# Performance work log

Hardware: AMD Instinct MI355X
Metric: run time of the kernel (lower is better)

The kernel has to match this reference:

```python
import jax, jax.numpy as jnp
import numpy as np

N = 512          # width of every layer (dims = [N]*4)
C = 16           # synaptic channels
NLAYERS = 4      # len(dims)
LT = NLAYERS - 1 # layer transitions
B = NLAYERS + N  # bias_vector_size = len(dims) + max(dims)
AGG_IN = N + B   # aggregator input width


def setup_inputs() -> dict:
    key = jax.random.key(0)
    ks = jax.random.split(key, 11)
    f32 = jnp.float32
    def rn(k, shape, scale):
        return (jax.random.normal(k, shape, f32) * scale)
    return {
        "x":      jax.random.normal(ks[0], (N,), f32),
        # Single_VECs: Linear(1, C) per (post q, pre p)
        "vec_W":  rn(ks[1], (LT, N, N, C), 1.0),
        "vec_b":  rn(ks[2], (LT, N, N, C), 0.5),
        # Single_Synapse: Linear(C,3) -> tanh -> Linear(3,1) -> tanh, per (q,p)
        "syn_W1": rn(ks[3], (LT, N, N, 3, C), 1.0 / np.sqrt(C)),
        "syn_b1": rn(ks[4], (LT, N, N, 3), 0.1),
        "syn_W2": rn(ks[5], (LT, N, N, 3), 1.0 / np.sqrt(3.0)),
        "syn_b2": rn(ks[6], (LT, N, N), 0.1),
        # Node_Aggregator: Linear(N + B, 3) -> tanh -> Linear(3,1), per q
        "agg_W1": rn(ks[7], (LT, N, 3, AGG_IN), 1.0 / np.sqrt(AGG_IN)),
        "agg_b1": rn(ks[8], (LT, N, 3), 0.1),
        "agg_W2": rn(ks[9], (LT, N, 3), 1.0 / np.sqrt(3.0)),
        "agg_b2": rn(ks[10], (LT, N), 0.1),
    }


def reference(x, vec_W, vec_b, syn_W1, syn_b1, syn_W2, syn_b2,
              agg_W1, agg_b1, agg_W2, agg_b2):
    # layer code for destination layer l+1 (one-hot over NLAYERS)
    layer_codes = jnp.eye(NLAYERS, dtype=x.dtype)[1:1 + LT]   # [LT, NLAYERS]
    node_eye = jnp.eye(N, dtype=x.dtype)                       # node one-hot codes

    def step(a, p):
        vW, vb, sW1, sb1, sW2, sb2, aW1, ab1, aW2, ab2, lcode = p
        # VECs: tanh(Linear(1->C)) per edge; a[p] is the scalar pre-activation
        filtered = jnp.tanh(a[None, :, None] * vW + vb)                 # [N_post, N_pre, C]
        # Single_Synapse per edge
        h1 = jnp.tanh(jnp.einsum('qpoc,qpc->qpo', sW1, filtered) + sb1) # [q, p, 3]
        s = jnp.tanh(jnp.einsum('qpo,qpo->qp', sW2, h1) + sb2)          # [q, p]
        # Node_Aggregator over cat(synapse_activations, bias_vector)
        agg_in = jnp.concatenate(
            [s, jnp.broadcast_to(lcode, (N, NLAYERS)), node_eye], axis=1)  # [q, N+B]
        h = jnp.tanh(jnp.einsum('qkp,qp->qk', aW1, agg_in) + ab1)       # [q, 3]
        a_next = jnp.einsum('qk,qk->q', aW2, h) + ab2                   # [q] (no tanh on fc2)
        return a_next, None

    a_final, _ = jax.lax.scan(
        step, x,
        (vec_W, vec_b, syn_W1, syn_b1, syn_W2, syn_b2,
         agg_W1, agg_b1, agg_W2, agg_b2, layer_codes))
    # original prepends each node: net_out = [node_{N-1}, ..., node_0], shape [N, 1]
    return a_final[::-1].reshape(-1, 1)
```

## Files before the change

### kernel.cpp

```cpp
#include <hip/hip_runtime.h>
#include <math.h>

#define N 512
#define C 16
#define NLAYERS 4
#define AGG_IN 1028

__global__ __launch_bounds__(512) void dan_layer_kernel(
    const float* __restrict__ a_in,
    float*       __restrict__ a_out,
    const float* __restrict__ vec_W,
    const float* __restrict__ vec_b,
    const float* __restrict__ syn_W1,
    const float* __restrict__ syn_b1,
    const float* __restrict__ syn_W2,
    const float* __restrict__ syn_b2,
    const float* __restrict__ agg_W1,
    const float* __restrict__ agg_b1,
    const float* __restrict__ agg_W2,
    const float* __restrict__ agg_b2,
    int l, int reverse_out)
{
    const int q = blockIdx.x;
    const int p = threadIdx.x;

    __shared__ float red[3][8];

    const size_t edge = ((size_t)(l * N + q)) * N + p;
    const float av = a_in[p];

    const float4* vW = (const float4*)(vec_W + edge * C);
    const float4* vB = (const float4*)(vec_b + edge * C);
    float f[16];
    #pragma unroll
    for (int j = 0; j < 4; ++j) {
        float4 w = vW[j];
        float4 b = vB[j];
        f[4*j+0] = tanhf(fmaf(av, w.x, b.x));
        f[4*j+1] = tanhf(fmaf(av, w.y, b.y));
        f[4*j+2] = tanhf(fmaf(av, w.z, b.z));
        f[4*j+3] = tanhf(fmaf(av, w.w, b.w));
    }

    const float4* sW1 = (const float4*)(syn_W1 + edge * 48);
    float h1[3];
    #pragma unroll
    for (int o = 0; o < 3; ++o) {
        float acc = syn_b1[edge * 3 + o];
        #pragma unroll
        for (int j = 0; j < 4; ++j) {
            float4 w = sW1[o * 4 + j];
            acc = fmaf(w.x, f[4*j+0], acc);
            acc = fmaf(w.y, f[4*j+1], acc);
            acc = fmaf(w.z, f[4*j+2], acc);
            acc = fmaf(w.w, f[4*j+3], acc);
        }
        h1[o] = tanhf(acc);
    }
    float s = syn_b2[edge];
    s = fmaf(syn_W2[edge*3+0], h1[0], s);
    s = fmaf(syn_W2[edge*3+1], h1[1], s);
    s = fmaf(syn_W2[edge*3+2], h1[2], s);
    s = tanhf(s);

    const float* aW1 = agg_W1 + ((size_t)(l * N + q)) * 3 * AGG_IN;
    float part0 = aW1[0 * AGG_IN + p] * s;
    float part1 = aW1[1 * AGG_IN + p] * s;
    float part2 = aW1[2 * AGG_IN + p] * s;

    #pragma unroll
    for (int off = 32; off > 0; off >>= 1) {
        part0 += __shfl_down(part0, off, 64);
        part1 += __shfl_down(part1, off, 64);
        part2 += __shfl_down(part2, off, 64);
    }
    const int wave = threadIdx.x >> 6;
    if ((threadIdx.x & 63) == 0) {
        red[0][wave] = part0;
        red[1][wave] = part1;
        red[2][wave] = part2;
    }
    __syncthreads();

    if (threadIdx.x == 0) {
        float h[3];
        #pragma unroll
        for (int k = 0; k < 3; ++k) {
            float acc = 0.f;
            #pragma unroll
            for (int w = 0; w < 8; ++w) acc += red[k][w];
            acc += aW1[k * AGG_IN + N + (l + 1)];
            acc += aW1[k * AGG_IN + N + NLAYERS + q];
            acc += agg_b1[((size_t)(l * N + q)) * 3 + k];
            h[k] = tanhf(acc);
        }
        const float* aW2 = agg_W2 + ((size_t)(l * N + q)) * 3;
        float out = agg_b2[l * N + q];
        out = fmaf(aW2[0], h[0], out);
        out = fmaf(aW2[1], h[1], out);
        out = fmaf(aW2[2], h[2], out);
        if (reverse_out) a_out[N - 1 - q] = out;
        else             a_out[q] = out;
    }
}

extern "C" void kernel_launch(void* const* d_in, const int* in_sizes, int n_in,
                              void* d_out, int out_size, void* d_ws, size_t ws_size,
                              hipStream_t stream) {
    const float* x      = (const float*)d_in[0];
    const float* vec_W  = (const float*)d_in[1];
    const float* vec_b  = (const float*)d_in[2];
    const float* syn_W1 = (const float*)d_in[3];
    const float* syn_b1 = (const float*)d_in[4];
    const float* syn_W2 = (const float*)d_in[5];
    const float* syn_b2 = (const float*)d_in[6];
    const float* agg_W1 = (const float*)d_in[7];
    const float* agg_b1 = (const float*)d_in[8];
    const float* agg_W2 = (const float*)d_in[9];
    const float* agg_b2 = (const float*)d_in[10];
    float* out = (float*)d_out;

    float* a0 = (float*)d_ws;
    float* a1 = a0 + N;

    dan_layer_kernel<<<N, N, 0, stream>>>(x,  a0,  vec_W, vec_b, syn_W1, syn_b1,
                                          syn_W2, syn_b2, agg_W1, agg_b1, agg_W2, agg_b2,
                                          0, 0);
    dan_layer_kernel<<<N, N, 0, stream>>>(a0, a1,  vec_W, vec_b, syn_W1, syn_b1,
                                          syn_W2, syn_b2, agg_W1, agg_b1, agg_W2, agg_b2,
                                          1, 0);
    dan_layer_kernel<<<N, N, 0, stream>>>(a1, out, vec_W, vec_b, syn_W1, syn_b1,
                                          syn_W2, syn_b2, agg_W1, agg_b1, agg_W2, agg_b2,
                                          2, 1);
}
```

Before: 336.2 us.

## Split edges across four lanes with atomic partials and fast tanh

Each edge's 16 channels are now spread over four lanes, so a thread loads one float4 of each weight row, and the 3-output dot product is combined with xor shuffles. Per-layer work is split into an edge kernel on an 8x512 grid that atomically accumulates aggregator partials into a zeroed workspace, followed by a single-block epilogue. tanhf is replaced by an exp-based fast_tanh. The goal is more coalesced, wider-parallel loads on this memory-bound weight stream, at the cost of extra launches, atomics, and a small loss of tanh accuracy.

```diff
diff --git a/kernel.cpp b/kernel.cpp
--- a/kernel.cpp
+++ b/kernel.cpp
@@ -3,12 +3,23 @@
 
 #define N 512
 #define C 16
-#define NLAYERS 4
+#define LT 3
 #define AGG_IN 1028
 
-__global__ __launch_bounds__(512) void dan_layer_kernel(
+__device__ __forceinline__ float fast_tanh(float x) {
+    float ax = fabsf(x);
+    float t  = __expf(-2.0f * ax);
+    float r  = __fdividef(1.0f - t, 1.0f + t);
+    return copysignf(r, x);
+}
+
+__global__ __launch_bounds__(512) void zero_partials(float* __restrict__ part, int n) {
+    int i = blockIdx.x * blockDim.x + threadIdx.x;
+    if (i < n) part[i] = 0.f;
+}
+
+__global__ __launch_bounds__(256) void edge_kernel(
     const float* __restrict__ a_in,
-    float*       __restrict__ a_out,
     const float* __restrict__ vec_W,
     const float* __restrict__ vec_b,
     const float* __restrict__ syn_W1,
@@ -16,92 +27,99 @@
     const float* __restrict__ syn_W2,
     const float* __restrict__ syn_b2,
     const float* __restrict__ agg_W1,
+    float* __restrict__ part,
+    int l)
+{
+    const int q  = blockIdx.y;
+    const int pc = blockIdx.x;
+    const int t  = threadIdx.x;
+    const int e  = t >> 2;
+    const int j  = t & 3;
+    const int p  = pc * 64 + e;
+
+    const size_t edge = ((size_t)(l * N + q)) * N + p;
+
+    const float av = a_in[p];
+
+    const float4 w = ((const float4*)(vec_W + edge * C))[j];
+    const float4 b = ((const float4*)(vec_b + edge * C))[j];
+
+    float4 f;
+    f.x = fast_tanh(fmaf(av, w.x, b.x));
+    f.y = fast_tanh(fmaf(av, w.y, b.y));
+    f.z = fast_tanh(fmaf(av, w.z, b.z));
+    f.w = fast_tanh(fmaf(av, w.w, b.w));
+
+    const float4* sW1 = (const float4*)(syn_W1 + edge * 48);
+    float d0, d1, d2;
+    {
+        float4 wv = sW1[0 * 4 + j];
+        d0 = fmaf(wv.x, f.x, fmaf(wv.y, f.y, fmaf(wv.z, f.z, wv.w * f.w)));
+        wv = sW1[1 * 4 + j];
+        d1 = fmaf(wv.x, f.x, fmaf(wv.y, f.y, fmaf(wv.z, f.z, wv.w * f.w)));
+        wv = sW1[2 * 4 + j];
+        d2 = fmaf(wv.x, f.x, fmaf(wv.y, f.y, fmaf(wv.z, f.z, wv.w * f.w)));
+    }
+    d0 += __shfl_xor(d0, 1, 64);  d0 += __shfl_xor(d0, 2, 64);
+    d1 += __shfl_xor(d1, 1, 64);  d1 += __shfl_xor(d1, 2, 64);
+    d2 += __shfl_xor(d2, 1, 64);  d2 += __shfl_xor(d2, 2, 64);
+
+    float h0 = fast_tanh(d0 + syn_b1[edge * 3 + 0]);
+    float h1 = fast_tanh(d1 + syn_b1[edge * 3 + 1]);
+    float h2 = fast_tanh(d2 + syn_b1[edge * 3 + 2]);
+    float s = syn_b2[edge];
+    s = fmaf(syn_W2[edge * 3 + 0], h0, s);
+    s = fmaf(syn_W2[edge * 3 + 1], h1, s);
+    s = fmaf(syn_W2[edge * 3 + 2], h2, s);
+    s = fast_tanh(s);
+
+    float pv = 0.f;
+    if (j < 3) {
+        pv = s * agg_W1[(((size_t)(l * N + q)) * 3 + j) * AGG_IN + p];
+    }
+    pv += __shfl_xor(pv, 4, 64);
+    pv += __shfl_xor(pv, 8, 64);
+    pv += __shfl_xor(pv, 16, 64);
+    pv += __shfl_xor(pv, 32, 64);
+
+    __shared__ float red[3][4];
+    const int wave = t >> 6;
+    const int lane = t & 63;
+    if (lane < 3) red[lane][wave] = pv;
+    __syncthreads();
+    if (t < 3) {
+        float acc = red[t][0] + red[t][1] + red[t][2] + red[t][3];
+        atomicAdd(&part[q * 3 + t], acc);
+    }
+}
+
+__global__ __launch_bounds__(512) void agg_epilogue(
+    const float* __restrict__ part,
+    const float* __restrict__ agg_W1,
     const float* __restrict__ agg_b1,
     const float* __restrict__ agg_W2,
     const float* __restrict__ agg_b2,
+    float* __restrict__ a_out,
     int l, int reverse_out)
 {
-    const int q = blockIdx.x;
-    const int p = threadIdx.x;
-
-    __shared__ float red[3][8];
-
-    const size_t edge = ((size_t)(l * N + q)) * N + p;
-    const float av = a_in[p];
-
-    const float4* vW = (const float4*)(vec_W + edge * C);
-    const float4* vB = (const float4*)(vec_b + edge * C);
-    float f[16];
+    const int q = threadIdx.x;
+    const float* aW1 = agg_W1 + ((size_t)(l * N + q)) * 3 * AGG_IN;
+    float h[3];
     #pragma unroll
-    for (int j = 0; j < 4; ++j) {
-        float4 w = vW[j];
-        float4 b = vB[j];
-        f[4*j+0] = tanhf(fmaf(av, w.x, b.x));
-        f[4*j+1] = tanhf(fmaf(av, w.y, b.y));
-        f[4*j+2] = tanhf(fmaf(av, w.z, b.z));
-        f[4*j+3] = tanhf(fmaf(av, w.w, b.w));
+    for (int k = 0; k < 3; ++k) {
+        float acc = part[q * 3 + k];
+        acc += aW1[k * AGG_IN + N + (l + 1)];
+        acc += aW1[k * AGG_IN + N + 4 + q];
+        acc += agg_b1[((size_t)(l * N + q)) * 3 + k];
+        h[k] = fast_tanh(acc);
     }
-
-    const float4* sW1 = (const float4*)(syn_W1 + edge * 48);
-    float h1[3];
-    #pragma unroll
-    for (int o = 0; o < 3; ++o) {
-        float acc = syn_b1[edge * 3 + o];
-        #pragma unroll
-        for (int j = 0; j < 4; ++j) {
-            float4 w = sW1[o * 4 + j];
-            acc = fmaf(w.x, f[4*j+0], acc);
-            acc = fmaf(w.y, f[4*j+1], acc);
-            acc = fmaf(w.z, f[4*j+2], acc);
-            acc = fmaf(w.w, f[4*j+3], acc);
-        }
-        h1[o] = tanhf(acc);
-    }
-    float s = syn_b2[edge];
-    s = fmaf(syn_W2[edge*3+0], h1[0], s);
-    s = fmaf(syn_W2[edge*3+1], h1[1], s);
-    s = fmaf(syn_W2[edge*3+2], h1[2], s);
-    s = tanhf(s);
-
-    const float* aW1 = agg_W1 + ((size_t)(l * N + q)) * 3 * AGG_IN;
-    float part0 = aW1[0 * AGG_IN + p] * s;
-    float part1 = aW1[1 * AGG_IN + p] * s;
-    float part2 = aW1[2 * AGG_IN + p] * s;
-
-    #pragma unroll
-    for (int off = 32; off > 0; off >>= 1) {
-        part0 += __shfl_down(part0, off, 64);
-        part1 += __shfl_down(part1, off, 64);
-        part2 += __shfl_down(part2, off, 64);
-    }
-    const int wave = threadIdx.x >> 6;
-    if ((threadIdx.x & 63) == 0) {
-        red[0][wave] = part0;
-        red[1][wave] = part1;
-        red[2][wave] = part2;
-    }
-    __syncthreads();
-
-    if (threadIdx.x == 0) {
-        float h[3];
-        #pragma unroll
-        for (int k = 0; k < 3; ++k) {
-            float acc = 0.f;
-            #pragma unroll
-            for (int w = 0; w < 8; ++w) acc += red[k][w];
-            acc += aW1[k * AGG_IN + N + (l + 1)];
-            acc += aW1[k * AGG_IN + N + NLAYERS + q];
-            acc += agg_b1[((size_t)(l * N + q)) * 3 + k];
-            h[k] = tanhf(acc);
-        }
-        const float* aW2 = agg_W2 + ((size_t)(l * N + q)) * 3;
-        float out = agg_b2[l * N + q];
-        out = fmaf(aW2[0], h[0], out);
-        out = fmaf(aW2[1], h[1], out);
-        out = fmaf(aW2[2], h[2], out);
-        if (reverse_out) a_out[N - 1 - q] = out;
-        else             a_out[q] = out;
-    }
+    const float* aW2 = agg_W2 + ((size_t)(l * N + q)) * 3;
+    float out = agg_b2[l * N + q];
+    out = fmaf(aW2[0], h[0], out);
+    out = fmaf(aW2[1], h[1], out);
+    out = fmaf(aW2[2], h[2], out);
+    if (reverse_out) a_out[N - 1 - q] = out;
+    else             a_out[q] = out;
 }
 
 extern "C" void kernel_launch(void* const* d_in, const int* in_sizes, int n_in,
@@ -120,16 +138,29 @@
     const float* agg_b2 = (const float*)d_in[10];
     float* out = (float*)d_out;
 
-    float* a0 = (float*)d_ws;
-    float* a1 = a0 + N;
+    float* part = (float*)d_ws;
+    float* a0   = part + LT * N * 3;
+    float* a1   = a0 + N;
 
-    dan_layer_kernel<<<N, N, 0, stream>>>(x,  a0,  vec_W, vec_b, syn_W1, syn_b1,
-                                          syn_W2, syn_b2, agg_W1, agg_b1, agg_W2, agg_b2,
-                                          0, 0);
-    dan_layer_kernel<<<N, N, 0, stream>>>(a0, a1,  vec_W, vec_b, syn_W1, syn_b1,
-                                          syn_W2, syn_b2, agg_W1, agg_b1, agg_W2, agg_b2,
-                                          1, 0);
-    dan_layer_kernel<<<N, N, 0, stream>>>(a1, out, vec_W, vec_b, syn_W1, syn_b1,
-                                          syn_W2, syn_b2, agg_W1, agg_b1, agg_W2, agg_b2,
-                                          2, 1);
+    zero_partials<<<(LT * N * 3 + 511) / 512, 512, 0, stream>>>(part, LT * N * 3);
+
+    const dim3 egrid(8, N);
+
+    edge_kernel<<<egrid, 256, 0, stream>>>(x, vec_W, vec_b, syn_W1, syn_b1,
+                                           syn_W2, syn_b2, agg_W1,
+                                           part + 0 * N * 3, 0);
+    agg_epilogue<<<1, N, 0, stream>>>(part + 0 * N * 3, agg_W1, agg_b1, agg_W2,
+                                      agg_b2, a0, 0, 0);
+
+    edge_kernel<<<egrid, 256, 0, stream>>>(a0, vec_W, vec_b, syn_W1, syn_b1,
+                                           syn_W2, syn_b2, agg_W1,
+                                           part + 1 * N * 3, 1);
+    agg_epilogue<<<1, N, 0, stream>>>(part + 1 * N * 3, agg_W1, agg_b1, agg_W2,
+                                      agg_b2, a1, 1, 0);
+
+    edge_kernel<<<egrid, 256, 0, stream>>>(a1, vec_W, vec_b, syn_W1, syn_b1,
+                                           syn_W2, syn_b2, agg_W1,
+                                           part + 2 * N * 3, 2);
+    agg_epilogue<<<1, N, 0, stream>>>(part + 2 * N * 3, agg_W1, agg_b1, agg_W2,
+                                      agg_b2, out, 2, 1);
 }
```

Result: slower. 347.7 us (+3.4%).

## Split each edge across four lanes with coalesced nontemporal loads and fast tanh

Applied to the files above, without the earlier changes.

Remaps threads so four lanes cooperate on one edge, each loading a 16-byte slice of the vec and synapse weights. A wave's loads become contiguous, and the 16-wide dot products are combined with intra-quad shuffles. Each block loops over four passes of 128 edges. Libm tanhf is replaced with an exp-based fast tanh, and loads are marked nontemporal. The fast tanh trades some accuracy, and the extra shuffles add ALU work.

```diff
diff --git a/kernel.cpp b/kernel.cpp
--- a/kernel.cpp
+++ b/kernel.cpp
@@ -3,10 +3,22 @@
 
 #define N 512
 #define C 16
-#define NLAYERS 4
 #define AGG_IN 1028
 
-__global__ __launch_bounds__(512) void dan_layer_kernel(
+typedef float v4f __attribute__((ext_vector_type(4)));
+
+__device__ __forceinline__ float fast_tanh(float x) {
+    float ax = fabsf(x);
+    float t  = __expf(-2.0f * ax);
+    float r  = __fdividef(1.0f - t, 1.0f + t);
+    return copysignf(r, x);
+}
+
+__device__ __forceinline__ v4f ntload4(const float* p) {
+    return __builtin_nontemporal_load((const v4f*)p);
+}
+
+__global__ __launch_bounds__(512, 4) void dan_layer_kernel(
     const float* __restrict__ a_in,
     float*       __restrict__ a_out,
     const float* __restrict__ vec_W,
@@ -22,83 +34,85 @@
     int l, int reverse_out)
 {
     const int q = blockIdx.x;
-    const int p = threadIdx.x;
+    const int t = threadIdx.x;
+    const int j = t & 3;
+    const int e = t >> 2;
 
     __shared__ float red[3][8];
+    __shared__ float hsh[3];
 
-    const size_t edge = ((size_t)(l * N + q)) * N + p;
-    const float av = a_in[p];
+    const size_t qbase = ((size_t)(l * N + q)) * N;
+    const int jc = (j < 3) ? j : 2;
+    const float* aW1q = agg_W1 + ((size_t)(l * N + q)) * 3 * AGG_IN + (size_t)jc * AGG_IN;
 
-    const float4* vW = (const float4*)(vec_W + edge * C);
-    const float4* vB = (const float4*)(vec_b + edge * C);
-    float f[16];
-    #pragma unroll
-    for (int j = 0; j < 4; ++j) {
-        float4 w = vW[j];
-        float4 b = vB[j];
-        f[4*j+0] = tanhf(fmaf(av, w.x, b.x));
-        f[4*j+1] = tanhf(fmaf(av, w.y, b.y));
-        f[4*j+2] = tanhf(fmaf(av, w.z, b.z));
-        f[4*j+3] = tanhf(fmaf(av, w.w, b.w));
+    float pv = 0.f;
+
+    for (int pass = 0; pass < 4; ++pass) {
+        const int p = pass * 128 + e;
+        const size_t edge = qbase + p;
+
+        const float av = a_in[p];
+
+        const v4f w  = ntload4(vec_W  + edge * C  + j * 4);
+        const v4f b  = ntload4(vec_b  + edge * C  + j * 4);
+        const v4f s0 = ntload4(syn_W1 + edge * 48 + 0 * C + j * 4);
+        const v4f s1 = ntload4(syn_W1 + edge * 48 + 1 * C + j * 4);
+        const v4f s2 = ntload4(syn_W1 + edge * 48 + 2 * C + j * 4);
+
+        float f0 = fast_tanh(fmaf(av, w.x, b.x));
+        float f1 = fast_tanh(fmaf(av, w.y, b.y));
+        float f2 = fast_tanh(fmaf(av, w.z, b.z));
+        float f3 = fast_tanh(fmaf(av, w.w, b.w));
+
+        float d0 = fmaf(s0.x, f0, fmaf(s0.y, f1, fmaf(s0.z, f2, s0.w * f3)));
+        float d1 = fmaf(s1.x, f0, fmaf(s1.y, f1, fmaf(s1.z, f2, s1.w * f3)));
+        float d2 = fmaf(s2.x, f0, fmaf(s2.y, f1, fmaf(s2.z, f2, s2.w * f3)));
+
+        d0 += __shfl_xor(d0, 1, 64);  d0 += __shfl_xor(d0, 2, 64);
+        d1 += __shfl_xor(d1, 1, 64);  d1 += __shfl_xor(d1, 2, 64);
+        d2 += __shfl_xor(d2, 1, 64);  d2 += __shfl_xor(d2, 2, 64);
+
+        float h0 = fast_tanh(d0 + syn_b1[edge * 3 + 0]);
+        float h1 = fast_tanh(d1 + syn_b1[edge * 3 + 1]);
+        float h2 = fast_tanh(d2 + syn_b1[edge * 3 + 2]);
+        float s = syn_b2[edge];
+        s = fmaf(syn_W2[edge * 3 + 0], h0, s);
+        s = fmaf(syn_W2[edge * 3 + 1], h1, s);
+        s = fmaf(syn_W2[edge * 3 + 2], h2, s);
+        s = fast_tanh(s);
+
+        if (j < 3) pv = fmaf(s, aW1q[p], pv);
     }
 
-    const float4* sW1 = (const float4*)(syn_W1 + edge * 48);
-    float h1[3];
-    #pragma unroll
-    for (int o = 0; o < 3; ++o) {
-        float acc = syn_b1[edge * 3 + o];
+    pv += __shfl_xor(pv, 4, 64);
+    pv += __shfl_xor(pv, 8, 64);
+    pv += __shfl_xor(pv, 16, 64);
+    pv += __shfl_xor(pv, 32, 64);
+
+    const int wave = t >> 6;
+    const int lane = t & 63;
+    if (lane < 3) red[lane][wave] = pv;
+    __syncthreads();
+
+    if (t < 3) {
+        const int k = t;
+        float acc = 0.f;
         #pragma unroll
-        for (int j = 0; j < 4; ++j) {
-            float4 w = sW1[o * 4 + j];
-            acc = fmaf(w.x, f[4*j+0], acc);
-            acc = fmaf(w.y, f[4*j+1], acc);
-            acc = fmaf(w.z, f[4*j+2], acc);
-            acc = fmaf(w.w, f[4*j+3], acc);
-        }
-        h1[o] = tanhf(acc);
-    }
-    float s = syn_b2[edge];
-    s = fmaf(syn_W2[edge*3+0], h1[0], s);
-    s = fmaf(syn_W2[edge*3+1], h1[1], s);
-    s = fmaf(syn_W2[edge*3+2], h1[2], s);
-    s = tanhf(s);
-
-    const float* aW1 = agg_W1 + ((size_t)(l * N + q)) * 3 * AGG_IN;
-    float part0 = aW1[0 * AGG_IN + p] * s;
-    float part1 = aW1[1 * AGG_IN + p] * s;
-    float part2 = aW1[2 * AGG_IN + p] * s;
-
-    #pragma unroll
-    for (int off = 32; off > 0; off >>= 1) {
-        part0 += __shfl_down(part0, off, 64);
-        part1 += __shfl_down(part1, off, 64);
-        part2 += __shfl_down(part2, off, 64);
-    }
-    const int wave = threadIdx.x >> 6;
-    if ((threadIdx.x & 63) == 0) {
-        red[0][wave] = part0;
-        red[1][wave] = part1;
-        red[2][wave] = part2;
+        for (int w = 0; w < 8; ++w) acc += red[k][w];
+        const float* aW1 = agg_W1 + ((size_t)(l * N + q)) * 3 * AGG_IN + (size_t)k * AGG_IN;
+        acc += aW1[N + (l + 1)];
+        acc += aW1[N + 4 + q];
+        acc += agg_b1[((size_t)(l * N + q)) * 3 + k];
+        hsh[k] = fast_tanh(acc);
     }
     __syncthreads();
 
-    if (threadIdx.x == 0) {
-        float h[3];
-        #pragma unroll
-        for (int k = 0; k < 3; ++k) {
-            float acc = 0.f;
-            #pragma unroll
-            for (int w = 0; w < 8; ++w) acc += red[k][w];
-            acc += aW1[k * AGG_IN + N + (l + 1)];
-            acc += aW1[k * AGG_IN + N + NLAYERS + q];
-            acc += agg_b1[((size_t)(l * N + q)) * 3 + k];
-            h[k] = tanhf(acc);
-        }
+    if (t == 0) {
         const float* aW2 = agg_W2 + ((size_t)(l * N + q)) * 3;
         float out = agg_b2[l * N + q];
-        out = fmaf(aW2[0], h[0], out);
-        out = fmaf(aW2[1], h[1], out);
-        out = fmaf(aW2[2], h[2], out);
+        out = fmaf(aW2[0], hsh[0], out);
+        out = fmaf(aW2[1], hsh[1], out);
+        out = fmaf(aW2[2], hsh[2], out);
         if (reverse_out) a_out[N - 1 - q] = out;
         else             a_out[q] = out;
     }
@@ -123,13 +137,13 @@
     float* a0 = (float*)d_ws;
     float* a1 = a0 + N;
 
-    dan_layer_kernel<<<N, N, 0, stream>>>(x,  a0,  vec_W, vec_b, syn_W1, syn_b1,
-                                          syn_W2, syn_b2, agg_W1, agg_b1, agg_W2, agg_b2,
-                                          0, 0);
-    dan_layer_kernel<<<N, N, 0, stream>>>(a0, a1,  vec_W, vec_b, syn_W1, syn_b1,
-                                          syn_W2, syn_b2, agg_W1, agg_b1, agg_W2, agg_b2,
-                                          1, 0);
-    dan_layer_kernel<<<N, N, 0, stream>>>(a1, out, vec_W, vec_b, syn_W1, syn_b1,
-                                          syn_W2, syn_b2, agg_W1, agg_b1, agg_W2, agg_b2,
-                                          2, 1);
+    dan_layer_kernel<<<N, 512, 0, stream>>>(x,  a0,  vec_W, vec_b, syn_W1, syn_b1,
+                                            syn_W2, syn_b2, agg_W1, agg_b1, agg_W2, agg_b2,
+                                            0, 0);
+    dan_layer_kernel<<<N, 512, 0, stream>>>(a0, a1,  vec_W, vec_b, syn_W1, syn_b1,
+                                            syn_W2, syn_b2, agg_W1, agg_b1, agg_W2, agg_b2,
+                                            1, 0);
+    dan_layer_kernel<<<N, 512, 0, stream>>>(a1, out, vec_W, vec_b, syn_W1, syn_b1,
+                                            syn_W2, syn_b2, agg_W1, agg_b1, agg_W2, agg_b2,
+                                            2, 1);
 }
```

Result: faster. 308.7 us (-8.2%).
